# Kernel tuning notes

Measured on AMD Instinct MI355X. Metric: run time of the kernel, lower is better.

The kernel has to match this reference:

```python
import jax, jax.numpy as jnp
import numpy as np

S = 3136        # tokens (56x56 patch grid, single image segment -> full attention)
H = 16          # num_heads
D = 80          # head_dim (= head_dim_ori = PADDING_HEAD_DIM)
HID = H * D     # 1280
SCALE = 1.0 / float(np.sqrt(D))  # qkScale = 1/sqrt(head_dim_ori)


def _rope_tables(s, d, base=10000.0):
    # rotate_half style: cos/sin of shape [s, d], duplicated over the two halves
    half = d // 2
    inv_freq = 1.0 / (base ** (np.arange(0, half, dtype=np.float32) / half))
    freqs = np.outer(np.arange(s, dtype=np.float32), inv_freq)  # [s, d/2]
    emb = np.concatenate([freqs, freqs], axis=-1)               # [s, d]
    return jnp.asarray(np.cos(emb)), jnp.asarray(np.sin(emb))


def setup_inputs() -> dict:
    key = jax.random.key(0)
    ks = jax.random.split(key, 6)
    cos, sin = _rope_tables(S, D)
    return {
        "hidden_states": jax.random.normal(ks[0], (S, HID), jnp.float32),
        "x_norm": jax.random.normal(ks[1], (S, HID), jnp.float32),
        "qkv_w": jax.random.normal(ks[2], (3 * HID, HID), jnp.float32) * 0.02,
        "qkv_b": jax.random.normal(ks[3], (3 * HID,), jnp.float32) * 0.02,
        "proj_w": jax.random.normal(ks[4], (HID, HID), jnp.float32) * 0.02,
        "proj_b": jax.random.normal(ks[5], (HID,), jnp.float32) * 0.02,
        "cos": cos,
        "sin": sin,
    }


def _rotate_half(x):
    x1, x2 = jnp.split(x, 2, axis=-1)
    return jnp.concatenate([-x2, x1], axis=-1)


def reference(hidden_states, x_norm, qkv_w, qkv_b, proj_w, proj_b, cos, sin):
    # fused QKV linear (transposeB=True) + split into q,k,v along last dim
    qkv = x_norm @ qkv_w.T + qkv_b                      # [S, 3*HID]
    q, k, v = jnp.split(qkv, 3, axis=-1)                # each [S, HID]
    q = q.reshape(S, H, D)
    k = k.reshape(S, H, D)
    v = v.reshape(S, H, D)
    # inline RoPE on q and k (rotate_half over full head_dim)
    c = cos[:, None, :]; s = sin[:, None, :]           # [S,1,D]
    q = q * c + _rotate_half(q) * s
    k = k * c + _rotate_half(k) * s
    # full self-attention (PA_ENCODER, single segment = seq_len S)
    scores = jnp.einsum('shd,thd->hst', q, k) * SCALE   # [H,S,S]
    probs = jax.nn.softmax(scores, axis=-1)
    attn = jnp.einsum('hst,thd->shd', probs, v)         # [S,H,D]
    attn = attn.reshape(S, HID)
    # output projection + residual add
    out = attn @ proj_w.T + proj_b
    return hidden_states + out
```

## Files before the change

### kernel.cpp

```cpp
#include <hip/hip_runtime.h>
#include <hip/hip_bf16.h>

#define S_   3136
#define H_   16
#define D_   80
#define DP_  96
#define HID_ 1280

typedef short  bf16x8 __attribute__((ext_vector_type(8)));
typedef short  bf16x4 __attribute__((ext_vector_type(4)));
typedef float  f32x4  __attribute__((ext_vector_type(4)));

__device__ __forceinline__ float b2f(unsigned short u) {
    union { unsigned int i; float f; } c;
    c.i = ((unsigned int)u) << 16;
    return c.f;
}
__device__ __forceinline__ unsigned short f2b(float f) {
    union { unsigned int i; float f; } c;
    c.f = f;
    unsigned int x = c.i;
    unsigned int lsb = (x >> 16) & 1u;
    x += 0x7fffu + lsb;
    return (unsigned short)(x >> 16);
}
__device__ __forceinline__ unsigned int cvt_pk_bf16(float lo, float hi) {
    unsigned int r;
    asm("v_cvt_pk_bf16_f32 %0, %1, %2" : "=v"(r) : "v"(lo), "v"(hi));
    return r;
}
__device__ __forceinline__ float exp2_hw(float x) {
    float r;
    asm("v_exp_f32 %0, %1" : "=v"(r) : "v"(x));
    return r;
}

typedef const void __attribute__((address_space(1))) GAS;
typedef void __attribute__((address_space(3))) LAS;
__device__ __forceinline__ void gl16(const void* g, void* l) {
    __builtin_amdgcn_global_load_lds((GAS*)g, (LAS*)l, 16, 0, 0);
}

#define N4_X 1003520
#define N4_Q 1228800
#define N4_P 409600

__global__ __launch_bounds__(256)
void cast3_kernel(const float* __restrict__ x0, unsigned short* __restrict__ y0,
                  const float* __restrict__ x1, unsigned short* __restrict__ y1,
                  const float* __restrict__ x2, unsigned short* __restrict__ y2)
{
    int i = blockIdx.x * 256 + threadIdx.x;
    const float* src; unsigned short* dst;
    if (i < N4_X)               { src = x0; dst = y0; }
    else if (i < N4_X + N4_Q)   { src = x1; dst = y1; i -= N4_X; }
    else if (i < N4_X + N4_Q + N4_P) { src = x2; dst = y2; i -= N4_X + N4_Q; }
    else return;
    float4 v = ((const float4*)src)[i];
    ushort4 o;
    o.x = f2b(v.x); o.y = f2b(v.y); o.z = f2b(v.z); o.w = f2b(v.w);
    ((ushort4*)dst)[i] = o;
}

#define ASTR 40

__global__ __launch_bounds__(256)
void qkv_mfma_kernel(const unsigned short* __restrict__ Ab,
                     const unsigned short* __restrict__ Wb,
                     const float* __restrict__ bias,
                     unsigned short* __restrict__ qo, unsigned short* __restrict__ ko,
                     unsigned short* __restrict__ vtb)
{
    __shared__ __align__(16) short As[2][128][ASTR];
    __shared__ __align__(16) short Bs[2][128][ASTR];
    int m0 = blockIdx.x * 128;
    int n0 = blockIdx.y * 128;
    int t = threadIdx.x;
    int wave = t >> 6, lane = t & 63, lq = lane & 15, quad = lane >> 4;
    int wr = wave >> 1, wc = wave & 1;

    int r0  = t >> 2;
    int r1  = r0 + 64;
    int kc0 = (t & 3) << 3;
    const unsigned short* pa0 = Ab + (size_t)min(m0 + r0, S_ - 1) * HID_ + kc0;
    const unsigned short* pa1 = Ab + (size_t)min(m0 + r1, S_ - 1) * HID_ + kc0;
    const unsigned short* pb0 = Wb + (size_t)(n0 + r0) * HID_ + kc0;
    const unsigned short* pb1 = Wb + (size_t)(n0 + r1) * HID_ + kc0;

    const bf16x8* afp[2][4]; const bf16x8* bfp[2][4];
    #pragma unroll
    for (int s = 0; s < 2; ++s)
        #pragma unroll
        for (int i = 0; i < 4; ++i) {
            afp[s][i] = (const bf16x8*)&As[s][wr * 64 + i * 16 + lq][quad * 8];
            bfp[s][i] = (const bf16x8*)&Bs[s][wc * 64 + i * 16 + lq][quad * 8];
        }

    f32x4 acc[4][4];
    #pragma unroll
    for (int i = 0; i < 4; ++i)
        #pragma unroll
        for (int j = 0; j < 4; ++j) acc[i][j] = (f32x4){0.f, 0.f, 0.f, 0.f};

    bf16x8 va[2][2], vb[2][2];
    #pragma unroll
    for (int s = 0; s < 2; ++s) {
        va[s][0] = *(const bf16x8*)(pa0 + s * 32);
        va[s][1] = *(const bf16x8*)(pa1 + s * 32);
        vb[s][0] = *(const bf16x8*)(pb0 + s * 32);
        vb[s][1] = *(const bf16x8*)(pb1 + s * 32);
    }

    for (int kt = 0; kt < HID_; kt += 64) {
        __syncthreads();
        #pragma unroll
        for (int s = 0; s < 2; ++s) {
            *(bf16x8*)&As[s][r0][kc0] = va[s][0];
            *(bf16x8*)&As[s][r1][kc0] = va[s][1];
            *(bf16x8*)&Bs[s][r0][kc0] = vb[s][0];
            *(bf16x8*)&Bs[s][r1][kc0] = vb[s][1];
        }
        __syncthreads();
        if (kt + 64 < HID_) {
            #pragma unroll
            for (int s = 0; s < 2; ++s) {
                va[s][0] = *(const bf16x8*)(pa0 + kt + 64 + s * 32);
                va[s][1] = *(const bf16x8*)(pa1 + kt + 64 + s * 32);
                vb[s][0] = *(const bf16x8*)(pb0 + kt + 64 + s * 32);
                vb[s][1] = *(const bf16x8*)(pb1 + kt + 64 + s * 32);
            }
        }
        #pragma unroll
        for (int s = 0; s < 2; ++s) {
            bf16x8 af[4], bfr[4];
            #pragma unroll
            for (int i = 0; i < 4; ++i) af[i]  = *afp[s][i];
            #pragma unroll
            for (int j = 0; j < 4; ++j) bfr[j] = *bfp[s][j];
            #pragma unroll
            for (int i = 0; i < 4; ++i)
                #pragma unroll
                for (int j = 0; j < 4; ++j)
                    acc[i][j] = __builtin_amdgcn_mfma_f32_16x16x32_bf16(af[i], bfr[j], acc[i][j], 0, 0, 0);
        }
    }

    #pragma unroll
    for (int i = 0; i < 4; ++i)
        #pragma unroll
        for (int j = 0; j < 4; ++j)
            #pragma unroll
            for (int reg = 0; reg < 4; ++reg) {
                int row = m0 + wr * 64 + i * 16 + quad * 4 + reg;
                if (row >= S_) continue;
                int col = n0 + wc * 64 + j * 16 + lq;
                float val = acc[i][j][reg] + bias[col];
                int which = col / HID_;
                int rem   = col - which * HID_;
                int h     = rem / D_;
                int d     = rem - h * D_;
                if (which == 0)      qo[((size_t)h * S_ + row) * D_ + d] = f2b(val);
                else if (which == 1) ko[((size_t)h * S_ + row) * D_ + d] = f2b(val);
                else                 vtb[((size_t)h * D_ + d) * S_ + row] = f2b(val);
            }
}

__global__ __launch_bounds__(256)
void proj_mfma_kernel(const unsigned short* __restrict__ Ab,
                      const unsigned short* __restrict__ Wb,
                      const float* __restrict__ bias, const float* __restrict__ hidden,
                      float* __restrict__ out)
{
    __shared__ __align__(16) short As[64][ASTR];
    __shared__ __align__(16) short Bs[64][ASTR];
    int m0 = blockIdx.x * 64;
    int n0 = blockIdx.y * 64;
    int t = threadIdx.x;
    int wave = t >> 6, lane = t & 63, lq = lane & 15, quad = lane >> 4;
    int wr = wave >> 1, wc = wave & 1;

    int r  = t >> 2;
    int kc0 = (t & 3) << 3;
    const unsigned short* pa = Ab + (size_t)(m0 + r) * HID_ + kc0;
    const unsigned short* pb = Wb + (size_t)(n0 + r) * HID_ + kc0;
    short* sa = &As[r][kc0];
    short* sb = &Bs[r][kc0];

    const bf16x8* afp[2]; const bf16x8* bfp[2];
    #pragma unroll
    for (int i = 0; i < 2; ++i) {
        afp[i] = (const bf16x8*)&As[wr * 32 + i * 16 + lq][quad * 8];
        bfp[i] = (const bf16x8*)&Bs[wc * 32 + i * 16 + lq][quad * 8];
    }

    f32x4 acc[2][2];
    #pragma unroll
    for (int i = 0; i < 2; ++i)
        #pragma unroll
        for (int j = 0; j < 2; ++j) acc[i][j] = (f32x4){0.f, 0.f, 0.f, 0.f};

    bf16x8 va = *(const bf16x8*)(pa);
    bf16x8 vb = *(const bf16x8*)(pb);

    for (int kt = 0; kt < HID_; kt += 32) {
        __syncthreads();
        *(bf16x8*)sa = va;
        *(bf16x8*)sb = vb;
        __syncthreads();
        if (kt + 32 < HID_) {
            va = *(const bf16x8*)(pa + kt + 32);
            vb = *(const bf16x8*)(pb + kt + 32);
        }
        bf16x8 af[2], bfr[2];
        #pragma unroll
        for (int i = 0; i < 2; ++i) af[i]  = *afp[i];
        #pragma unroll
        for (int j = 0; j < 2; ++j) bfr[j] = *bfp[j];
        #pragma unroll
        for (int i = 0; i < 2; ++i)
            #pragma unroll
            for (int j = 0; j < 2; ++j)
                acc[i][j] = __builtin_amdgcn_mfma_f32_16x16x32_bf16(af[i], bfr[j], acc[i][j], 0, 0, 0);
    }

    #pragma unroll
    for (int i = 0; i < 2; ++i)
        #pragma unroll
        for (int j = 0; j < 2; ++j)
            #pragma unroll
            for (int reg = 0; reg < 4; ++reg) {
                int row = m0 + wr * 32 + i * 16 + quad * 4 + reg;
                int col = n0 + wc * 32 + j * 16 + lq;
                out[(size_t)row * HID_ + col] =
                    acc[i][j][reg] + bias[col] + hidden[(size_t)row * HID_ + col];
            }
}

__global__ void rope_kernel(const unsigned short* __restrict__ q, const unsigned short* __restrict__ k,
                            const float* __restrict__ cost, const float* __restrict__ sint,
                            unsigned short* __restrict__ qb, unsigned short* __restrict__ kb)
{
    const float QSCALE = 0.11180339887498949f * 1.4426950408889634f;
    int idx = blockIdx.x * 256 + threadIdx.x;
    const int total = H_ * S_ * 40;
    if (idx >= total) return;
    int d  = idx % 40;
    int hs = idx / 40;
    int s  = hs % S_;
    size_t base  = (size_t)hs * D_;
    size_t base9 = (size_t)hs * DP_;
    float c1 = cost[s * D_ + d];
    float s1 = sint[s * D_ + d];
    float c2 = cost[s * D_ + d + 40];
    float s2 = sint[s * D_ + d + 40];
    float x1 = b2f(q[base + d]), x2 = b2f(q[base + d + 40]);
    qb[base9 + d]      = f2b((x1 * c1 - x2 * s1) * QSCALE);
    qb[base9 + d + 40] = f2b((x2 * c2 + x1 * s2) * QSCALE);
    x1 = b2f(k[base + d]); x2 = b2f(k[base + d + 40]);
    kb[base9 + d]      = f2b(x1 * c1 - x2 * s1);
    kb[base9 + d + 40] = f2b(x2 * c2 + x1 * s2);
    if (d < 16) {
        qb[base9 + 80 + d] = 0;
        kb[base9 + 80 + d] = 0;
    }
}

#define KBUF_ 16384
#define VBUF_ 10240
#define BUF_  26624

__global__ __launch_bounds__(256, 3)
void attn_kernel(const unsigned short* __restrict__ Qb,
                 const unsigned short* __restrict__ Kb,
                 const unsigned short* __restrict__ Vtb,
                 unsigned short* __restrict__ attnb)
{
    __shared__ __align__(16) unsigned char smem[2 * BUF_];

    int h   = blockIdx.y;
    int qb0 = blockIdx.x * 64;
    int t      = threadIdx.x;
    int wave   = t >> 6;
    int lane   = t & 63;
    int lq     = lane & 15;
    int quad   = lane >> 4;
    int qh     = wave & 1;
    int stripe = wave >> 1;
    int Q0     = qb0 + qh * 32;
    int swz    = (lq & 7) << 4;

    bf16x8 qf[2][3];
    #pragma unroll
    for (int qt = 0; qt < 2; ++qt)
        #pragma unroll
        for (int kc = 0; kc < 3; ++kc)
            qf[qt][kc] = *(const bf16x8*)(Qb + ((size_t)h * S_ + Q0 + qt * 16 + lq) * DP_ + kc * 32 + quad * 8);

    f32x4 O[2][5];
    #pragma unroll
    for (int qt = 0; qt < 2; ++qt)
        #pragma unroll
        for (int dt = 0; dt < 5; ++dt) O[qt][dt] = (f32x4){0.f, 0.f, 0.f, 0.f};
    float l_acc[2] = {0.f, 0.f};

    const unsigned char* kS[4]; int kD[4];
    #pragma unroll
    for (int ii = 0; ii < 4; ++ii) {
        int i  = wave * 4 + ii;
        int rl = i * 4 + (lane >> 4);
        kS[ii] = (const unsigned char*)(Kb + ((size_t)h * S_ + rl) * DP_)
               + (((lane & 15) * 16) ^ ((rl & 7) << 4));
        kD[ii] = i * 1024;
    }
    const unsigned char* vS[3]; int vD[3];
    int nv = (wave < 2) ? 3 : 2;
    #pragma unroll
    for (int jj = 0; jj < 3; ++jj) {
        int j = (jj < 2) ? (wave + jj * 4) : (8 + wave);
        int d = j * 8 + (lane >> 3);
        vS[jj] = (const unsigned char*)(Vtb + (size_t)(h * D_ + d) * S_)
               + (((lane & 7) * 16) ^ ((d & 7) << 4));
        vD[jj] = KBUF_ + j * 1024;
    }

    #define STAGE(bufoff, rr)                                                   \
        do {                                                                    \
            size_t kadv = (size_t)(rr) * (64 * DP_ * 2);                        \
            size_t vadv = (size_t)(rr) * 128;                                   \
            _Pragma("unroll")                                                   \
            for (int ii = 0; ii < 4; ++ii)                                      \
                gl16(kS[ii] + kadv, smem + (bufoff) + kD[ii]);                  \
            _Pragma("unroll")                                                   \
            for (int jj = 0; jj < 3; ++jj)                                      \
                if (jj < nv) gl16(vS[jj] + vadv, smem + (bufoff) + vD[jj]);     \
        } while (0)

    STAGE(0, 0);
    asm volatile("s_waitcnt vmcnt(0)" ::: "memory");
    __syncthreads();

    int cur = 0;
    for (int r = 0; r < 49; ++r) {
        if (r < 48) STAGE(cur ^ BUF_, r + 1);

        const unsigned char* Kbase = smem + cur;
        const unsigned char* Vbase = Kbase + KBUF_;

        f32x4 sc[2][2];
        __builtin_amdgcn_s_setprio(1);
        #pragma unroll
        for (int kt = 0; kt < 2; ++kt) {
            const unsigned char* kbp = Kbase + (stripe * 32 + kt * 16 + lq) * 256;
            bf16x8 kf0 = *(const bf16x8*)(kbp + ((  0 + quad * 16) ^ swz));
            bf16x8 kf1 = *(const bf16x8*)(kbp + (( 64 + quad * 16) ^ swz));
            bf16x8 kf2 = *(const bf16x8*)(kbp + ((128 + quad * 16) ^ swz));
            #pragma unroll
            for (int qt = 0; qt < 2; ++qt) {
                f32x4 a = (f32x4){0.f, 0.f, 0.f, 0.f};
                a = __builtin_amdgcn_mfma_f32_16x16x32_bf16(kf0, qf[qt][0], a, 0, 0, 0);
                a = __builtin_amdgcn_mfma_f32_16x16x32_bf16(kf1, qf[qt][1], a, 0, 0, 0);
                a = __builtin_amdgcn_mfma_f32_16x16x32_bf16(kf2, qf[qt][2], a, 0, 0, 0);
                sc[qt][kt] = a;
            }
        }
        __builtin_amdgcn_s_setprio(0);

        union PaU { bf16x8 v8; unsigned int d[4]; } pa[2];
        #pragma unroll
        for (int qt = 0; qt < 2; ++qt) {
            float e00 = exp2_hw(sc[qt][0][0]), e01 = exp2_hw(sc[qt][0][1]);
            float e02 = exp2_hw(sc[qt][0][2]), e03 = exp2_hw(sc[qt][0][3]);
            float e10 = exp2_hw(sc[qt][1][0]), e11 = exp2_hw(sc[qt][1][1]);
            float e12 = exp2_hw(sc[qt][1][2]), e13 = exp2_hw(sc[qt][1][3]);
            l_acc[qt] += ((e00 + e01) + (e02 + e03)) + ((e10 + e11) + (e12 + e13));
            pa[qt].d[0] = cvt_pk_bf16(e00, e01);
            pa[qt].d[1] = cvt_pk_bf16(e02, e03);
            pa[qt].d[2] = cvt_pk_bf16(e10, e11);
            pa[qt].d[3] = cvt_pk_bf16(e12, e13);
        }

        __builtin_amdgcn_s_setprio(1);
        #pragma unroll
        for (int dt = 0; dt < 5; ++dt) {
            const unsigned char* vbp = Vbase + (dt * 16 + lq) * 128;
            union { bf16x8 v8; bf16x4 v4[2]; } vv;
            vv.v4[0] = *(const bf16x4*)(vbp + ((stripe * 64 +      quad * 8) ^ swz));
            vv.v4[1] = *(const bf16x4*)(vbp + ((stripe * 64 + 32 + quad * 8) ^ swz));
            #pragma unroll
            for (int qt = 0; qt < 2; ++qt)
                O[qt][dt] = __builtin_amdgcn_mfma_f32_16x16x32_bf16(pa[qt].v8, vv.v8, O[qt][dt], 0, 0, 0);
        }
        __builtin_amdgcn_s_setprio(0);

        asm volatile("s_waitcnt vmcnt(0)" ::: "memory");
        __syncthreads();
        cur ^= BUF_;
    }
    #undef STAGE

    float lr[2];
    #pragma unroll
    for (int qt = 0; qt < 2; ++qt) {
        float l = l_acc[qt];
        l += __shfl_xor(l, 16);
        l += __shfl_xor(l, 32);
        lr[qt] = l;
    }
    f32x4* Of = (f32x4*)smem;
    float* Lf = (float*)(smem + 20480);
    if (stripe == 1) {
        #pragma unroll
        for (int qt = 0; qt < 2; ++qt) {
            #pragma unroll
            for (int dt = 0; dt < 5; ++dt)
                Of[((qh * 2 + qt) * 5 + dt) * 64 + lane] = O[qt][dt];
            if (lane < 16) Lf[(qh * 2 + qt) * 16 + lane] = lr[qt];
        }
    }
    __syncthreads();
    if (stripe == 0) {
        #pragma unroll
        for (int qt = 0; qt < 2; ++qt) {
            float ltot = lr[qt] + Lf[(qh * 2 + qt) * 16 + lq];
            #pragma unroll
            for (int dt = 0; dt < 5; ++dt)
                O[qt][dt] += Of[((qh * 2 + qt) * 5 + dt) * 64 + lane];
            #pragma unroll
            for (int reg = 0; reg < 4; ++reg) {
                float l = __shfl(ltot, quad * 4 + reg, 16);
                float linv = 1.0f / l;
                int s = Q0 + qt * 16 + quad * 4 + reg;
                unsigned short* orow = attnb + (size_t)s * HID_ + h * D_;
                #pragma unroll
                for (int dt = 0; dt < 5; ++dt)
                    orow[dt * 16 + lq] = f2b(O[qt][dt][reg] * linv);
            }
        }
    }
}

extern "C" void kernel_launch(void* const* d_in, const int* in_sizes, int n_in,
                              void* d_out, int out_size, void* d_ws, size_t ws_size,
                              hipStream_t stream)
{
    const float* hidden = (const float*)d_in[0];
    const float* x_norm = (const float*)d_in[1];
    const float* qkv_w  = (const float*)d_in[2];
    const float* qkv_b  = (const float*)d_in[3];
    const float* proj_w = (const float*)d_in[4];
    const float* proj_b = (const float*)d_in[5];
    const float* cost   = (const float*)d_in[6];
    const float* sint   = (const float*)d_in[7];
    float* out = (float*)d_out;

    unsigned short* w      = (unsigned short*)d_ws;
    unsigned short* qbuf   = w;
    unsigned short* kbuf   = qbuf + 4014080;
    unsigned short* vtb    = kbuf + 4014080;
    unsigned short* kbb    = vtb + 4064256;
    unsigned short* xb     = kbb + 4816896;
    unsigned short* wqkvb  = xb + 4014080;
    unsigned short* wprojb = wqkvb + 4915200;
    unsigned short* qbb    = wqkvb;
    unsigned short* abuf   = qbuf;

    cast3_kernel<<<(N4_X + N4_Q + N4_P + 255) / 256, 256, 0, stream>>>(
        x_norm, xb, qkv_w, wqkvb, proj_w, wprojb);

    qkv_mfma_kernel<<<dim3(25, 30), 256, 0, stream>>>(xb, wqkvb, qkv_b, qbuf, kbuf, vtb);
    rope_kernel<<<(H_ * S_ * 40 + 255) / 256, 256, 0, stream>>>(qbuf, kbuf, cost, sint, qbb, kbb);
    attn_kernel<<<dim3(S_ / 64, H_), 256, 0, stream>>>(qbb, kbb, vtb, abuf);
    proj_mfma_kernel<<<dim3(49, 20), 256, 0, stream>>>(abuf, wprojb, proj_b, hidden, out);
}
```

Baseline: 299.5 us.

## Use direct global-to-LDS loads in QKV GEMM and vectorize RoPE kernel

The QKV GEMM replaces its register-staged global loads and LDS stores with a gl16 helper that copies 16-byte chunks straight into double-buffered LDS. The next K-slice is prefetched while MFMAs run on the current buffer. The RoPE kernel now handles 8 elements per thread with 16-byte vector loads and stores instead of one element pair per thread, which cuts the thread count and the scalar memory operations. Risks: the unpadded 64-byte LDS rows may cause bank conflicts on the fragment reads, and the full vmcnt waits limit overlap.

```diff
diff --git a/kernel.cpp b/kernel.cpp
--- a/kernel.cpp
+++ b/kernel.cpp
@@ -62,8 +62,6 @@
     ((ushort4*)dst)[i] = o;
 }
 
-#define ASTR 40
-
 __global__ __launch_bounds__(256)
 void qkv_mfma_kernel(const unsigned short* __restrict__ Ab,
                      const unsigned short* __restrict__ Wb,
@@ -71,30 +69,33 @@
                      unsigned short* __restrict__ qo, unsigned short* __restrict__ ko,
                      unsigned short* __restrict__ vtb)
 {
-    __shared__ __align__(16) short As[2][128][ASTR];
-    __shared__ __align__(16) short Bs[2][128][ASTR];
+    __shared__ __align__(16) short As[2][128][32];
+    __shared__ __align__(16) short Bs[2][128][32];
     int m0 = blockIdx.x * 128;
     int n0 = blockIdx.y * 128;
     int t = threadIdx.x;
     int wave = t >> 6, lane = t & 63, lq = lane & 15, quad = lane >> 4;
     int wr = wave >> 1, wc = wave & 1;
 
-    int r0  = t >> 2;
-    int r1  = r0 + 64;
-    int kc0 = (t & 3) << 3;
-    const unsigned short* pa0 = Ab + (size_t)min(m0 + r0, S_ - 1) * HID_ + kc0;
-    const unsigned short* pa1 = Ab + (size_t)min(m0 + r1, S_ - 1) * HID_ + kc0;
-    const unsigned short* pb0 = Wb + (size_t)(n0 + r0) * HID_ + kc0;
-    const unsigned short* pb1 = Wb + (size_t)(n0 + r1) * HID_ + kc0;
-
-    const bf16x8* afp[2][4]; const bf16x8* bfp[2][4];
-    #pragma unroll
-    for (int s = 0; s < 2; ++s)
-        #pragma unroll
-        for (int i = 0; i < 4; ++i) {
-            afp[s][i] = (const bf16x8*)&As[s][wr * 64 + i * 16 + lq][quad * 8];
-            bfp[s][i] = (const bf16x8*)&Bs[s][wc * 64 + i * 16 + lq][quad * 8];
-        }
+    const unsigned short* aS[2]; const unsigned short* bS[2]; int dD[2];
+    #pragma unroll
+    for (int ii = 0; ii < 2; ++ii) {
+        int i   = wave * 2 + ii;
+        int row = i * 16 + (lane >> 2);
+        int kc  = (lane & 3) * 8;
+        aS[ii] = Ab + (size_t)min(m0 + row, S_ - 1) * HID_ + kc;
+        bS[ii] = Wb + (size_t)(n0 + row) * HID_ + kc;
+        dD[ii] = i * 1024;
+    }
+
+    #define QSTAGE(buf, kk)                                                     \
+        do {                                                                    \
+            _Pragma("unroll")                                                   \
+            for (int ii = 0; ii < 2; ++ii) {                                    \
+                gl16(aS[ii] + (kk), (char*)As + (buf) * 8192 + dD[ii]);         \
+                gl16(bS[ii] + (kk), (char*)Bs + (buf) * 8192 + dD[ii]);         \
+            }                                                                   \
+        } while (0)
 
     f32x4 acc[4][4];
     #pragma unroll
@@ -102,48 +103,41 @@
         #pragma unroll
         for (int j = 0; j < 4; ++j) acc[i][j] = (f32x4){0.f, 0.f, 0.f, 0.f};
 
-    bf16x8 va[2][2], vb[2][2];
-    #pragma unroll
-    for (int s = 0; s < 2; ++s) {
-        va[s][0] = *(const bf16x8*)(pa0 + s * 32);
-        va[s][1] = *(const bf16x8*)(pa1 + s * 32);
-        vb[s][0] = *(const bf16x8*)(pb0 + s * 32);
-        vb[s][1] = *(const bf16x8*)(pb1 + s * 32);
-    }
+    #define QCOMPUTE(buf)                                                       \
+        do {                                                                    \
+            bf16x8 af[4], bfr[4];                                               \
+            _Pragma("unroll")                                                   \
+            for (int i = 0; i < 4; ++i)                                         \
+                af[i] = *(const bf16x8*)((const char*)As + (buf) * 8192         \
+                        + (wr * 64 + i * 16 + lq) * 64 + quad * 16);            \
+            _Pragma("unroll")                                                   \
+            for (int j = 0; j < 4; ++j)                                         \
+                bfr[j] = *(const bf16x8*)((const char*)Bs + (buf) * 8192        \
+                        + (wc * 64 + j * 16 + lq) * 64 + quad * 16);            \
+            _Pragma("unroll")                                                   \
+            for (int i = 0; i < 4; ++i)                                         \
+                _Pragma("unroll")                                               \
+                for (int j = 0; j < 4; ++j)                                     \
+                    acc[i][j] = __builtin_amdgcn_mfma_f32_16x16x32_bf16(        \
+                        af[i], bfr[j], acc[i][j], 0, 0, 0);                     \
+        } while (0)
+
+    QSTAGE(0, 0);
+    asm volatile("s_waitcnt vmcnt(0)" ::: "memory");
+    __syncthreads();
 
     for (int kt = 0; kt < HID_; kt += 64) {
+        QSTAGE(1, kt + 32);
+        QCOMPUTE(0);
+        asm volatile("s_waitcnt vmcnt(0)" ::: "memory");
         __syncthreads();
-        #pragma unroll
-        for (int s = 0; s < 2; ++s) {
-            *(bf16x8*)&As[s][r0][kc0] = va[s][0];
-            *(bf16x8*)&As[s][r1][kc0] = va[s][1];
-            *(bf16x8*)&Bs[s][r0][kc0] = vb[s][0];
-            *(bf16x8*)&Bs[s][r1][kc0] = vb[s][1];
-        }
+        if (kt + 64 < HID_) QSTAGE(0, kt + 64);
+        QCOMPUTE(1);
+        asm volatile("s_waitcnt vmcnt(0)" ::: "memory");
         __syncthreads();
-        if (kt + 64 < HID_) {
-            #pragma unroll
-            for (int s = 0; s < 2; ++s) {
-                va[s][0] = *(const bf16x8*)(pa0 + kt + 64 + s * 32);
-                va[s][1] = *(const bf16x8*)(pa1 + kt + 64 + s * 32);
-                vb[s][0] = *(const bf16x8*)(pb0 + kt + 64 + s * 32);
-                vb[s][1] = *(const bf16x8*)(pb1 + kt + 64 + s * 32);
-            }
-        }
-        #pragma unroll
-        for (int s = 0; s < 2; ++s) {
-            bf16x8 af[4], bfr[4];
-            #pragma unroll
-            for (int i = 0; i < 4; ++i) af[i]  = *afp[s][i];
-            #pragma unroll
-            for (int j = 0; j < 4; ++j) bfr[j] = *bfp[s][j];
-            #pragma unroll
-            for (int i = 0; i < 4; ++i)
-                #pragma unroll
-                for (int j = 0; j < 4; ++j)
-                    acc[i][j] = __builtin_amdgcn_mfma_f32_16x16x32_bf16(af[i], bfr[j], acc[i][j], 0, 0, 0);
-        }
-    }
+    }
+    #undef QSTAGE
+    #undef QCOMPUTE
 
     #pragma unroll
     for (int i = 0; i < 4; ++i)
@@ -165,6 +159,8 @@
             }
 }
 
+#define ASTR 40
+
 __global__ __launch_bounds__(256)
 void proj_mfma_kernel(const unsigned short* __restrict__ Ab,
                       const unsigned short* __restrict__ Wb,
@@ -236,32 +232,57 @@
             }
 }
 
-__global__ void rope_kernel(const unsigned short* __restrict__ q, const unsigned short* __restrict__ k,
-                            const float* __restrict__ cost, const float* __restrict__ sint,
-                            unsigned short* __restrict__ qb, unsigned short* __restrict__ kb)
+__global__ __launch_bounds__(256)
+void rope_kernel(const unsigned short* __restrict__ q, const unsigned short* __restrict__ k,
+                 const float* __restrict__ cost, const float* __restrict__ sint,
+                 unsigned short* __restrict__ qb, unsigned short* __restrict__ kb)
 {
     const float QSCALE = 0.11180339887498949f * 1.4426950408889634f;
     int idx = blockIdx.x * 256 + threadIdx.x;
-    const int total = H_ * S_ * 40;
+    const int total = H_ * S_ * 5;
     if (idx >= total) return;
-    int d  = idx % 40;
-    int hs = idx / 40;
+    int j  = idx % 5;
+    int hs = idx / 5;
     int s  = hs % S_;
-    size_t base  = (size_t)hs * D_;
-    size_t base9 = (size_t)hs * DP_;
-    float c1 = cost[s * D_ + d];
-    float s1 = sint[s * D_ + d];
-    float c2 = cost[s * D_ + d + 40];
-    float s2 = sint[s * D_ + d + 40];
-    float x1 = b2f(q[base + d]), x2 = b2f(q[base + d + 40]);
-    qb[base9 + d]      = f2b((x1 * c1 - x2 * s1) * QSCALE);
-    qb[base9 + d + 40] = f2b((x2 * c2 + x1 * s2) * QSCALE);
-    x1 = b2f(k[base + d]); x2 = b2f(k[base + d + 40]);
-    kb[base9 + d]      = f2b(x1 * c1 - x2 * s1);
-    kb[base9 + d + 40] = f2b(x2 * c2 + x1 * s2);
-    if (d < 16) {
-        qb[base9 + 80 + d] = 0;
-        kb[base9 + 80 + d] = 0;
+    int d0 = j * 8;
+    const unsigned short* qp = q + (size_t)hs * D_ + d0;
+    const unsigned short* kp = k + (size_t)hs * D_ + d0;
+    unsigned short* qo = qb + (size_t)hs * DP_ + d0;
+    unsigned short* ko = kb + (size_t)hs * DP_ + d0;
+    const float* cp = cost + s * D_ + d0;
+    const float* sp = sint + s * D_ + d0;
+
+    bf16x8 q1 = *(const bf16x8*)(qp);
+    bf16x8 q2 = *(const bf16x8*)(qp + 40);
+    bf16x8 k1 = *(const bf16x8*)(kp);
+    bf16x8 k2 = *(const bf16x8*)(kp + 40);
+    f32x4 c1[2] = { *(const f32x4*)(cp),      *(const f32x4*)(cp + 4)  };
+    f32x4 c2[2] = { *(const f32x4*)(cp + 40), *(const f32x4*)(cp + 44) };
+    f32x4 s1[2] = { *(const f32x4*)(sp),      *(const f32x4*)(sp + 4)  };
+    f32x4 s2[2] = { *(const f32x4*)(sp + 40), *(const f32x4*)(sp + 44) };
+
+    bf16x8 oq1, oq2, ok1, ok2;
+    #pragma unroll
+    for (int e = 0; e < 8; ++e) {
+        float cc1 = c1[e >> 2][e & 3], ss1 = s1[e >> 2][e & 3];
+        float cc2 = c2[e >> 2][e & 3], ss2 = s2[e >> 2][e & 3];
+        float x1 = b2f((unsigned short)q1[e]), x2 = b2f((unsigned short)q2[e]);
+        oq1[e] = (short)f2b((x1 * cc1 - x2 * ss1) * QSCALE);
+        oq2[e] = (short)f2b((x2 * cc2 + x1 * ss2) * QSCALE);
+        x1 = b2f((unsigned short)k1[e]); x2 = b2f((unsigned short)k2[e]);
+        ok1[e] = (short)f2b(x1 * cc1 - x2 * ss1);
+        ok2[e] = (short)f2b(x2 * cc2 + x1 * ss2);
+    }
+    *(bf16x8*)(qo)      = oq1;
+    *(bf16x8*)(qo + 40) = oq2;
+    *(bf16x8*)(ko)      = ok1;
+    *(bf16x8*)(ko + 40) = ok2;
+    if (j == 0) {
+        uint4 z = {0u, 0u, 0u, 0u};
+        *(uint4*)(qo + 80) = z;
+        *(uint4*)(qo + 88) = z;
+        *(uint4*)(ko + 80) = z;
+        *(uint4*)(ko + 88) = z;
     }
 }
 
@@ -468,7 +489,7 @@
         x_norm, xb, qkv_w, wqkvb, proj_w, wprojb);
 
     qkv_mfma_kernel<<<dim3(25, 30), 256, 0, stream>>>(xb, wqkvb, qkv_b, qbuf, kbuf, vtb);
-    rope_kernel<<<(H_ * S_ * 40 + 255) / 256, 256, 0, stream>>>(qbuf, kbuf, cost, sint, qbb, kbb);
+    rope_kernel<<<(H_ * S_ * 5 + 255) / 256, 256, 0, stream>>>(qbuf, kbuf, cost, sint, qbb, kbb);
     attn_kernel<<<dim3(S_ / 64, H_), 256, 0, stream>>>(qbb, kbb, vtb, abuf);
     proj_mfma_kernel<<<dim3(49, 20), 256, 0, stream>>>(abuf, wprojb, proj_b, hidden, out);
 }
```

Result: slower. 319.9 us (+6.8%).
